# Kernel tuning notes

Hardware: AMD Instinct MI355X
Metric: run time of the kernel (lower is better)

The kernel has to match this reference:

```python
import jax, jax.numpy as jnp
import numpy as np

B, N, FD = 2, 50000, 13
E = 250000
M, H = 128, 128          # message_dim, hidden_dim
EDGE_IN = 2 * FD + 8     # 34
NODE_IN = FD + 2 * M     # 269


def _mlp(x, w1, b1, w2, b2):
    return jnp.tanh(x @ w1 + b1) @ w2 + b2


def setup_inputs() -> dict:
    root = jax.random.key(0)
    k = lambda i: jax.random.fold_in(root, i)

    def lin(i, din, dout):
        w = jax.random.normal(k(i), (din, dout), jnp.float32) * np.float32(1.0 / np.sqrt(din))
        b = jax.random.normal(k(i + 100), (dout,), jnp.float32) * np.float32(0.01)
        return w, b

    ew1, eb1 = lin(1, EDGE_IN, H); ew2, eb2 = lin(2, H, M)      # mlp_edge
    ww1, wb1 = lin(3, EDGE_IN, H); ww2, wb2 = lin(4, H, 1)      # mlp_weight
    xw1, xb1 = lin(5, EDGE_IN, H); xw2, xb2 = lin(6, H, M)      # mlp_edge_world
    yw1, yb1 = lin(7, EDGE_IN, H); yw2, yb2 = lin(8, H, 1)      # mlp_weight_world
    nw1, nb1 = lin(9, NODE_IN, H); nw2, nb2 = lin(10, H, FD)    # mlp_node

    z_h = jax.random.normal(k(20), (B, N, FD), jnp.float32)
    edge_hh = jax.random.randint(k(21), (B, 2, E), 0, N, jnp.int32)
    edge_world = jax.random.randint(k(22), (B, 2, E), 0, N, jnp.int32)
    return dict(z_h=z_h, edge_hh=edge_hh, edge_world=edge_world,
                ew1=ew1, eb1=eb1, ew2=ew2, eb2=eb2,
                ww1=ww1, wb1=wb1, ww2=ww2, wb2=wb2,
                xw1=xw1, xb1=xb1, xw2=xw2, xb2=xb2,
                yw1=yw1, yb1=yb1, yw2=yw2, yb2=yb2,
                nw1=nw1, nb1=nb1, nw2=nw2, nb2=nb2)


def _edge_features(z, s, t):
    # z: (N, FD); s, t: (E,)
    pos, vel = z[:, 0:3], z[:, 3:6]
    diff = pos[s] - pos[t]                               # (E, 3)
    dist = jnp.sum(diff * diff, axis=-1, keepdims=True)  # (E, 1) squared distance
    vxc = jnp.cross(vel[s], vel[t])                      # (E, 3)
    vxn = jnp.linalg.norm(vxc, axis=-1, keepdims=True)   # (E, 1)
    return jnp.concatenate([diff, dist, vxc, vxn], axis=-1)  # (E, 8)


def reference(z_h, edge_hh, edge_world,
              ew1, eb1, ew2, eb2, ww1, wb1, ww2, wb2,
              xw1, xb1, xw2, xb2, yw1, yb1, yw2, yb2,
              nw1, nb1, nw2, nb2):
    n_nodes = z_h.shape[1]

    def per_batch(z, e_hh, e_w):
        # normal edges
        s, t = e_hh[0], e_hh[1]
        inp = jnp.concatenate([z[s], z[t], _edge_features(z, s, t)], axis=-1)  # (E, 34)
        m = _mlp(inp, ew1, eb1, ew2, eb2)                                       # (E, M)
        w = jax.nn.sigmoid(_mlp(inp, ww1, wb1, ww2, wb2))                       # (E, 1)
        agg_h = jnp.zeros((n_nodes, M), z.dtype).at[t].add(w * m)
        # world edges
        sw, tw = e_w[0], e_w[1]
        inpw = jnp.concatenate([z[sw], z[tw], _edge_features(z, sw, tw)], axis=-1)
        mw = _mlp(inpw, xw1, xb1, xw2, xb2)
        ww_ = jax.nn.sigmoid(_mlp(inpw, yw1, yb1, yw2, yb2))
        agg_w = jnp.zeros((n_nodes, M), z.dtype).at[tw].add(ww_ * mw)
        return agg_h, agg_w

    m_agg_h, m_agg_w = jax.vmap(per_batch)(z_h, edge_hh, edge_world)  # (B, N, M) each
    input_node = jnp.concatenate([z_h, m_agg_h, m_agg_w], axis=-1)    # (B, N, 269)
    delta_z_h = _mlp(input_node, nw1, nb1, nw2, nb2)                  # (B, N, 13)
    return delta_z_h
```

## Files before the change

kernel.cpp:

```cpp
#include <hip/hip_runtime.h>
#include <hip/hip_bf16.h>

#define B_   2
#define N_   50000
#define FD_  13
#define E_   250000
#define M_   128
#define H_   128

typedef __attribute__((ext_vector_type(8))) short  short8;
typedef __attribute__((ext_vector_type(8))) __bf16 bf16x8;
typedef __attribute__((ext_vector_type(4))) float  f32x4;
typedef __attribute__((ext_vector_type(8))) unsigned short ushort8;

#define MSG_BYTES  (4ull * E_ * 128 * 2)
#define HIST_BYTES (4ull * N_ * 4)
#define SORT_BYTES (4ull * E_ * 4)
#define OFF_EW1 0u
#define OFF_WW1 8192u
#define OFF_EW2 16384u
#define OFF_XW1 32768u
#define OFF_YW1 40960u
#define OFF_XW2 49152u
#define OFF_NW1 65536u
#define OFF_NW2 102400u

__device__ __forceinline__ float bf2f(unsigned short u) {
    unsigned int v = ((unsigned int)u) << 16;
    return __builtin_bit_cast(float, v);
}
__device__ __forceinline__ unsigned short f2bf(float f) {
    __bf16 h = (__bf16)f;
    return __builtin_bit_cast(unsigned short, h);
}
__device__ __forceinline__ float tanh_fast(float x) {
    float e = __expf(x + x);
    float r = __builtin_amdgcn_rcpf(e + 1.0f);
    return __builtin_fmaf(-2.0f, r, 1.0f);
}
__device__ __forceinline__ float sigmoid_fast(float x) {
    return __builtin_amdgcn_rcpf(1.0f + __expf(-x));
}
__device__ __forceinline__ f32x4 mfma16(short8 a, short8 b, f32x4 c) {
    return __builtin_amdgcn_mfma_f32_16x16x32_bf16(
        __builtin_bit_cast(bf16x8, a), __builtin_bit_cast(bf16x8, b), c, 0, 0, 0);
}

__global__ void prep_kernel(const float* __restrict__ ew1, const float* __restrict__ ww1,
                            const float* __restrict__ ew2, const float* __restrict__ xw1,
                            const float* __restrict__ yw1, const float* __restrict__ xw2,
                            const float* __restrict__ nw1, const float* __restrict__ nw2,
                            unsigned short* __restrict__ fb) {
    int m = blockIdx.y, f = blockIdx.x, l = threadIdx.x;
    const float* src; int K, Nn, KS; unsigned int off;
    switch (m) {
        case 0: src = ew1; K = 34;  Nn = 128; KS = 2; off = OFF_EW1; break;
        case 1: src = ww1; K = 34;  Nn = 128; KS = 2; off = OFF_WW1; break;
        case 2: src = ew2; K = 128; Nn = 128; KS = 4; off = OFF_EW2; break;
        case 3: src = xw1; K = 34;  Nn = 128; KS = 2; off = OFF_XW1; break;
        case 4: src = yw1; K = 34;  Nn = 128; KS = 2; off = OFF_YW1; break;
        case 5: src = xw2; K = 128; Nn = 128; KS = 4; off = OFF_XW2; break;
        case 6: src = nw1; K = 269; Nn = 128; KS = 9; off = OFF_NW1; break;
        default: src = nw2; K = 128; Nn = 13; KS = 4; off = OFF_NW2; break;
    }
    int NT = (Nn + 15) / 16;
    if (f >= KS * NT) return;
    int ks = f / NT, nt = f % NT;
    int n = nt * 16 + (l & 15);
    unsigned short* dst = fb + off + ((unsigned int)f * 64u + (unsigned int)l) * 8u;
    #pragma unroll
    for (int j = 0; j < 8; j++) {
        int k = ks * 32 + ((l >> 4) * 8) + j;
        int kk = k; bool valid = (k < K) && (n < Nn);
        if (m == 6) {
            if (k < 256)      kk = k + 13;
            else if (k < 269) kk = k - 256;
            else              valid = false;
            valid = valid && (n < Nn);
        }
        dst[j] = valid ? f2bf(src[kk * Nn + n]) : (unsigned short)0;
    }
}

__global__ void hist_kernel(const int* __restrict__ ehh, const int* __restrict__ eww,
                            int* __restrict__ hist) {
    int p = blockIdx.y, idx = blockIdx.x * 256 + threadIdx.x;
    if (idx >= E_) return;
    const int* eg = ((p >> 1) ? eww : ehh) + (size_t)(p & 1) * 2 * E_;
    atomicAdd(&hist[p * N_ + eg[E_ + idx]], 1);
}

__global__ void scan_kernel(int* __restrict__ hist) {
    __shared__ int part[1024];
    const int p = blockIdx.x, tid = threadIdx.x;
    int* h = hist + p * N_;
    const int lo = tid * 52;
    int cnt = N_ - lo; if (cnt < 0) cnt = 0; if (cnt > 52) cnt = 52;
    int v[52];
    int sum = 0;
    if (cnt == 52) {
        const int4* src = (const int4*)(h + lo);
        #pragma unroll
        for (int i = 0; i < 13; i++) {
            int4 t = src[i];
            v[4*i] = t.x; v[4*i+1] = t.y; v[4*i+2] = t.z; v[4*i+3] = t.w;
        }
        #pragma unroll
        for (int i = 0; i < 52; i++) sum += v[i];
    } else {
        for (int i = 0; i < cnt; i++) sum += h[lo + i];
    }
    part[tid] = sum;
    __syncthreads();
    for (int off = 1; off < 1024; off <<= 1) {
        int t = (tid >= off) ? part[tid - off] : 0;
        __syncthreads();
        part[tid] += t;
        __syncthreads();
    }
    int excl = (tid == 0) ? 0 : part[tid - 1];
    if (cnt == 52) {
        int4* dst = (int4*)(h + lo);
        #pragma unroll
        for (int i = 0; i < 13; i++) {
            int4 o;
            o.x = excl; excl += v[4*i];
            o.y = excl; excl += v[4*i+1];
            o.z = excl; excl += v[4*i+2];
            o.w = excl; excl += v[4*i+3];
            dst[i] = o;
        }
    } else {
        for (int i = 0; i < cnt; i++) { int t = h[lo + i]; h[lo + i] = excl; excl += t; }
    }
}

__global__ void scatter_kernel(const int* __restrict__ ehh, const int* __restrict__ eww,
                               int* __restrict__ hist, unsigned int* __restrict__ sorted) {
    int p = blockIdx.y, idx = blockIdx.x * 256 + threadIdx.x;
    if (idx >= E_) return;
    const int* eg = ((p >> 1) ? eww : ehh) + (size_t)(p & 1) * 2 * E_;
    int s = eg[idx];
    int t = eg[E_ + idx];
    int pos = atomicAdd(&hist[p * N_ + t], 1);
    sorted[(size_t)p * E_ + pos] = (unsigned int)s | ((unsigned int)t << 16);
}

__launch_bounds__(256, 3)
__global__ void edge_kernel_msg(const float* __restrict__ z,
                                const unsigned int* __restrict__ sorted,
                                const unsigned short* __restrict__ fb,
                                unsigned short* __restrict__ msg,
                                const float* __restrict__ eb1, const float* __restrict__ wb1,
                                const float* __restrict__ ww2, const float* __restrict__ wb2,
                                const float* __restrict__ eb2,
                                const float* __restrict__ xb1, const float* __restrict__ yb1,
                                const float* __restrict__ yw2, const float* __restrict__ yb2,
                                const float* __restrict__ xb2) {
    __shared__ alignas(16) unsigned short Abuf[128][48];
    __shared__ alignas(16) unsigned short Hbuf[128][136];
    __shared__ float w_acc[128];

    const int tid  = threadIdx.x;
    const int lane = tid & 63, wv = tid >> 6, quad = lane >> 4, c = lane & 15;
    const int pass = blockIdx.y, b = pass & 1, set = pass >> 1;
    const int ebase = blockIdx.x * 128;

    const float* zb = z + (size_t)b * N_ * FD_;
    unsigned short* msgp = msg + (size_t)pass * E_ * 128;

    const short8* Fm1 = (const short8*)(fb + (set ? OFF_XW1 : OFF_EW1));
    const short8* Fw1 = (const short8*)(fb + (set ? OFF_YW1 : OFF_WW1));
    const short8* Fm2 = (const short8*)(fb + (set ? OFF_XW2 : OFF_EW2));
    const float* B1m = set ? xb1 : eb1;
    const float* B1w = set ? yb1 : wb1;
    const float* B2m = set ? xb2 : eb2;
    const float* Wv2 = set ? yw2 : ww2;
    const float wbias = (set ? yb2 : wb2)[0];

    const int nt0 = wv * 2;
    short8 bm[2][2], bw[2][2], b2f[2][4];
    float bias1m[2], bias1w[2], bias2m[2], w2v[2];
    #pragma unroll
    for (int i = 0; i < 2; i++) {
        int nt = nt0 + i, n = nt * 16 + c;
        #pragma unroll
        for (int ks = 0; ks < 2; ks++) { bm[i][ks] = Fm1[(ks * 8 + nt) * 64 + lane];
                                         bw[i][ks] = Fw1[(ks * 8 + nt) * 64 + lane]; }
        #pragma unroll
        for (int ks = 0; ks < 4; ks++) { b2f[i][ks] = Fm2[(ks * 8 + nt) * 64 + lane]; }
        bias1m[i] = B1m[n]; bias1w[i] = B1w[n];
        bias2m[i] = B2m[n]; w2v[i] = Wv2[n];
    }

    if (tid < 128) {
        const int e = tid;
        int sp = ebase + e; if (sp >= E_) sp = E_ - 1;
        unsigned int st = sorted[(size_t)pass * E_ + sp];
        int s = (int)(st & 0xffffu), t = (int)(st >> 16);
        w_acc[e] = 0.0f;
        const float* zs = zb + (size_t)s * 13;
        const float* zt = zb + (size_t)t * 13;
        float fs[13], ft[13];
        __builtin_memcpy(fs, zs, 13 * sizeof(float));
        __builtin_memcpy(ft, zt, 13 * sizeof(float));
        float d0 = fs[0] - ft[0], d1 = fs[1] - ft[1], d2 = fs[2] - ft[2];
        float dist = d0 * d0 + d1 * d1 + d2 * d2;
        float c0 = fs[4] * ft[5] - fs[5] * ft[4];
        float c1 = fs[5] * ft[3] - fs[3] * ft[5];
        float c2 = fs[3] * ft[4] - fs[4] * ft[3];
        float vxn = sqrtf(c0 * c0 + c1 * c1 + c2 * c2);
        unsigned short row[40];
        #pragma unroll
        for (int j = 0; j < 13; j++) { row[j] = f2bf(fs[j]); row[13 + j] = f2bf(ft[j]); }
        row[26] = f2bf(d0); row[27] = f2bf(d1); row[28] = f2bf(d2); row[29] = f2bf(dist);
        row[30] = f2bf(c0); row[31] = f2bf(c1); row[32] = f2bf(c2); row[33] = f2bf(vxn);
        #pragma unroll
        for (int j = 34; j < 40; j++) row[j] = 0;
        #pragma unroll
        for (int v = 0; v < 5; v++) {
            short8 sv;
            #pragma unroll
            for (int j = 0; j < 8; j++) sv[j] = (short)row[v * 8 + j];
            *((short8*)&Abuf[e][v * 8]) = sv;
        }
    }
    __syncthreads();

    #pragma unroll 1
    for (int rt = 0; rt < 8; rt++) {
        const unsigned short* ar = &Abuf[rt * 16 + c][0];
        short8 a0 = *((const short8*)(ar + quad * 8));
        short8 a1 = {};
        if (quad == 0) a1 = *((const short8*)(ar + 32));
        float wpart[4] = {0.f, 0.f, 0.f, 0.f};
        #pragma unroll
        for (int i = 0; i < 2; i++) {
            f32x4 accm = {bias1m[i], bias1m[i], bias1m[i], bias1m[i]};
            f32x4 accw = {bias1w[i], bias1w[i], bias1w[i], bias1w[i]};
            accm = mfma16(a0, bm[i][0], accm);
            accm = mfma16(a1, bm[i][1], accm);
            accw = mfma16(a0, bw[i][0], accw);
            accw = mfma16(a1, bw[i][1], accw);
            int n = (nt0 + i) * 16 + c;
            #pragma unroll
            for (int r = 0; r < 4; r++) {
                Hbuf[rt * 16 + quad * 4 + r][n] = f2bf(tanh_fast(accm[r]));
                wpart[r] += tanh_fast(accw[r]) * w2v[i];
            }
        }
        #pragma unroll
        for (int r = 0; r < 4; r++) {
            float v = wpart[r];
            v += __shfl_xor(v, 1); v += __shfl_xor(v, 2);
            v += __shfl_xor(v, 4); v += __shfl_xor(v, 8);
            if (c == r) atomicAdd(&w_acc[rt * 16 + quad * 4 + r], v);
        }
    }
    __syncthreads();
    if (tid < 128) w_acc[tid] = sigmoid_fast(w_acc[tid] + wbias);
    __syncthreads();

    #pragma unroll 1
    for (int rt = 0; rt < 8; rt++) {
        const unsigned short* hr = &Hbuf[rt * 16 + c][0];
        short8 h0 = *((const short8*)(hr + quad * 8));
        short8 h1 = *((const short8*)(hr + 32 + quad * 8));
        short8 h2 = *((const short8*)(hr + 64 + quad * 8));
        short8 h3 = *((const short8*)(hr + 96 + quad * 8));
        const int elq = rt * 16 + quad * 4;
        const float g0 = w_acc[elq + 0], g1 = w_acc[elq + 1];
        const float g2 = w_acc[elq + 2], g3 = w_acc[elq + 3];
        #pragma unroll
        for (int i = 0; i < 2; i++) {
            f32x4 acc = {bias2m[i], bias2m[i], bias2m[i], bias2m[i]};
            acc = mfma16(h0, b2f[i][0], acc);
            acc = mfma16(h1, b2f[i][1], acc);
            acc = mfma16(h2, b2f[i][2], acc);
            acc = mfma16(h3, b2f[i][3], acc);
            const int n = (nt0 + i) * 16 + c;
            const float gv[4] = {g0, g1, g2, g3};
            #pragma unroll
            for (int r = 0; r < 4; r++) {
                int e = elq + r;
                if (ebase + e < E_)
                    msgp[(size_t)(ebase + e) * 128 + n] = f2bf(acc[r] * gv[r]);
            }
        }
    }
}

__launch_bounds__(256, 4)
__global__ void node_fused(const float* __restrict__ z,
                           const unsigned short* __restrict__ msg,
                           const int* __restrict__ hist,
                           const unsigned short* __restrict__ fb,
                           const float* __restrict__ nb1,
                           const float* __restrict__ nb2,
                           float* __restrict__ out) {
    __shared__ alignas(16) unsigned short Abuf[16][296];
    __shared__ alignas(16) unsigned short Hbuf[16][136];

    const int tid  = threadIdx.x;
    const int lane = tid & 63, wv = tid >> 6, quad = lane >> 4, c = lane & 15;
    const int g0 = blockIdx.x * 16;

    {
        const int nl = tid >> 4;
        const int part = tid & 15;
        const int g = g0 + nl;
        const int b = (g >= N_) ? 1 : 0;
        const int t = g - b * N_;
        #pragma unroll
        for (int s = 0; s < 2; s++) {
            const int p = s * 2 + b;
            const int end   = hist[p * N_ + t];
            const int start = (t > 0) ? hist[p * N_ + t - 1] : 0;
            float acc[8];
            #pragma unroll
            for (int k = 0; k < 8; k++) acc[k] = 0.f;
            const unsigned short* mp = msg + (size_t)p * E_ * 128 + part * 8;
            int j = start;
            for (; j + 8 <= end; j += 8) {
                ushort8 m[8];
                #pragma unroll
                for (int q = 0; q < 8; q++)
                    m[q] = *(const ushort8*)(mp + (size_t)(j + q) * 128);
                #pragma unroll
                for (int k = 0; k < 8; k++)
                    acc[k] += ((bf2f(m[0][k]) + bf2f(m[1][k])) + (bf2f(m[2][k]) + bf2f(m[3][k])))
                            + ((bf2f(m[4][k]) + bf2f(m[5][k])) + (bf2f(m[6][k]) + bf2f(m[7][k])));
            }
            for (; j + 2 <= end; j += 2) {
                ushort8 m0 = *(const ushort8*)(mp + (size_t)(j + 0) * 128);
                ushort8 m1 = *(const ushort8*)(mp + (size_t)(j + 1) * 128);
                #pragma unroll
                for (int k = 0; k < 8; k++) acc[k] += bf2f(m0[k]) + bf2f(m1[k]);
            }
            for (; j < end; j++) {
                ushort8 m = *(const ushort8*)(mp + (size_t)j * 128);
                #pragma unroll
                for (int k = 0; k < 8; k++) acc[k] += bf2f(m[k]);
            }
            ushort8 u;
            #pragma unroll
            for (int k = 0; k < 8; k++) u[k] = f2bf(acc[k]);
            *((ushort8*)&Abuf[nl][s * 128 + part * 8]) = u;
        }
    }
    for (int j = tid; j < 16 * 13; j += 256) {
        int nl = j / 13, k = j % 13;
        Abuf[nl][256 + k] = f2bf(z[(size_t)(g0 + nl) * 13 + k]);
    }
    for (int j = tid; j < 16 * 19; j += 256) {
        int nl = j / 19, k = j % 19;
        Abuf[nl][269 + k] = 0;
    }
    __syncthreads();

    {
        const short8* F1 = (const short8*)(fb + OFF_NW1);
        const int nt0 = wv * 2;
        const float b1a = nb1[nt0 * 16 + c];
        const float b1b = nb1[(nt0 + 1) * 16 + c];
        f32x4 acc0 = {b1a, b1a, b1a, b1a};
        f32x4 acc1 = {b1b, b1b, b1b, b1b};
        #pragma unroll
        for (int ks = 0; ks < 9; ks++) {
            short8 a = *((const short8*)(&Abuf[c][0] + ks * 32 + quad * 8));
            acc0 = mfma16(a, F1[(ks * 8 + nt0) * 64 + lane], acc0);
            acc1 = mfma16(a, F1[(ks * 8 + nt0 + 1) * 64 + lane], acc1);
        }
        #pragma unroll
        for (int r = 0; r < 4; r++) {
            Hbuf[quad * 4 + r][nt0 * 16 + c]       = f2bf(tanh_fast(acc0[r]));
            Hbuf[quad * 4 + r][(nt0 + 1) * 16 + c] = f2bf(tanh_fast(acc1[r]));
        }
    }
    __syncthreads();

    if (wv == 0) {
        const short8* F2 = (const short8*)(fb + OFF_NW2);
        const float bias2 = (c < 13) ? nb2[c] : 0.0f;
        f32x4 acc = {bias2, bias2, bias2, bias2};
        #pragma unroll
        for (int ks = 0; ks < 4; ks++) {
            short8 h = *((const short8*)(&Hbuf[c][0] + ks * 32 + quad * 8));
            acc = mfma16(h, F2[ks * 64 + lane], acc);
        }
        #pragma unroll
        for (int r = 0; r < 4; r++) {
            int g = g0 + quad * 4 + r;
            if (c < 13) out[(size_t)g * 13 + c] = acc[r];
        }
    }
}

extern "C" void kernel_launch(void* const* d_in, const int* in_sizes, int n_in,
                              void* d_out, int out_size, void* d_ws, size_t ws_size,
                              hipStream_t stream) {
    const float* z   = (const float*)d_in[0];
    const int* ehh   = (const int*)d_in[1];
    const int* eww   = (const int*)d_in[2];
    const float* ew1 = (const float*)d_in[3];
    const float* eb1 = (const float*)d_in[4];
    const float* ew2 = (const float*)d_in[5];
    const float* eb2 = (const float*)d_in[6];
    const float* ww1 = (const float*)d_in[7];
    const float* wb1 = (const float*)d_in[8];
    const float* ww2 = (const float*)d_in[9];
    const float* wb2 = (const float*)d_in[10];
    const float* xw1 = (const float*)d_in[11];
    const float* xb1 = (const float*)d_in[12];
    const float* xw2 = (const float*)d_in[13];
    const float* xb2 = (const float*)d_in[14];
    const float* yw1 = (const float*)d_in[15];
    const float* yb1 = (const float*)d_in[16];
    const float* yw2 = (const float*)d_in[17];
    const float* yb2 = (const float*)d_in[18];
    const float* nw1 = (const float*)d_in[19];
    const float* nb1 = (const float*)d_in[20];
    const float* nw2 = (const float*)d_in[21];
    const float* nb2 = (const float*)d_in[22];

    unsigned short* msg = (unsigned short*)d_ws;
    int* hist   = (int*)((char*)d_ws + MSG_BYTES);
    unsigned int* sorted = (unsigned int*)((char*)d_ws + MSG_BYTES + HIST_BYTES);
    unsigned short* frag = (unsigned short*)((char*)d_ws + MSG_BYTES + HIST_BYTES + SORT_BYTES);

    hipMemsetAsync(hist, 0, HIST_BYTES, stream);
    prep_kernel<<<dim3(72, 8), 64, 0, stream>>>(ew1, ww1, ew2, xw1, yw1, xw2, nw1, nw2, frag);
    hist_kernel<<<dim3((E_ + 255) / 256, 4), 256, 0, stream>>>(ehh, eww, hist);
    scan_kernel<<<4, 1024, 0, stream>>>(hist);
    scatter_kernel<<<dim3((E_ + 255) / 256, 4), 256, 0, stream>>>(ehh, eww, hist, sorted);
    edge_kernel_msg<<<dim3((E_ + 127) / 128, 4), 256, 0, stream>>>(
        z, sorted, frag, msg,
        eb1, wb1, ww2, wb2, eb2,
        xb1, yb1, yw2, yb2, xb2);
    node_fused<<<(B_ * N_) / 16, 256, 0, stream>>>(
        z, msg, hist, frag, nb1, nb2, (float*)d_out);
}
```

Before: 436.1 us.

## Aggregate edge messages via float atomics instead of materializing per-edge messages

The edge kernel no longer writes a bf16 message per edge for the node kernel to reduce by CSR segment. It now adds weighted messages straight into an fp32 per-node aggregation buffer with atomicAdd, first merging consecutive rows that share a target (edges are sorted by target). The node kernel just reads the aggregated rows. This avoids writing and re-reading the large message buffer, at the cost of zeroing a 100MB fp32 buffer, atomic contention, and nondeterministic summation order.

```diff
diff --git a/kernel.cpp b/kernel.cpp
--- a/kernel.cpp
+++ b/kernel.cpp
@@ -13,7 +13,7 @@
 typedef __attribute__((ext_vector_type(4))) float  f32x4;
 typedef __attribute__((ext_vector_type(8))) unsigned short ushort8;
 
-#define MSG_BYTES  (4ull * E_ * 128 * 2)
+#define AGG_BYTES  (4ull * N_ * 128 * 4)
 #define HIST_BYTES (4ull * N_ * 4)
 #define SORT_BYTES (4ull * E_ * 4)
 #define OFF_EW1 0u
@@ -147,10 +147,10 @@
 }
 
 __launch_bounds__(256, 3)
-__global__ void edge_kernel_msg(const float* __restrict__ z,
+__global__ void edge_kernel_agg(const float* __restrict__ z,
                                 const unsigned int* __restrict__ sorted,
                                 const unsigned short* __restrict__ fb,
-                                unsigned short* __restrict__ msg,
+                                float* __restrict__ agg,
                                 const float* __restrict__ eb1, const float* __restrict__ wb1,
                                 const float* __restrict__ ww2, const float* __restrict__ wb2,
                                 const float* __restrict__ eb2,
@@ -160,6 +160,7 @@
     __shared__ alignas(16) unsigned short Abuf[128][48];
     __shared__ alignas(16) unsigned short Hbuf[128][136];
     __shared__ float w_acc[128];
+    __shared__ int   tgt_s[128];
 
     const int tid  = threadIdx.x;
     const int lane = tid & 63, wv = tid >> 6, quad = lane >> 4, c = lane & 15;
@@ -167,7 +168,7 @@
     const int ebase = blockIdx.x * 128;
 
     const float* zb = z + (size_t)b * N_ * FD_;
-    unsigned short* msgp = msg + (size_t)pass * E_ * 128;
+    float* aggp = agg + (size_t)pass * N_ * 128;
 
     const short8* Fm1 = (const short8*)(fb + (set ? OFF_XW1 : OFF_EW1));
     const short8* Fw1 = (const short8*)(fb + (set ? OFF_YW1 : OFF_WW1));
@@ -195,9 +196,12 @@
 
     if (tid < 128) {
         const int e = tid;
-        int sp = ebase + e; if (sp >= E_) sp = E_ - 1;
+        int sp = ebase + e;
+        const bool valid = (sp < E_);
+        if (!valid) sp = E_ - 1;
         unsigned int st = sorted[(size_t)pass * E_ + sp];
         int s = (int)(st & 0xffffu), t = (int)(st >> 16);
+        tgt_s[e] = valid ? t : -1;
         w_acc[e] = 0.0f;
         const float* zs = zb + (size_t)s * 13;
         const float* zt = zb + (size_t)t * 13;
@@ -269,8 +273,8 @@
         short8 h2 = *((const short8*)(hr + 64 + quad * 8));
         short8 h3 = *((const short8*)(hr + 96 + quad * 8));
         const int elq = rt * 16 + quad * 4;
-        const float g0 = w_acc[elq + 0], g1 = w_acc[elq + 1];
-        const float g2 = w_acc[elq + 2], g3 = w_acc[elq + 3];
+        const int   tg[4] = {tgt_s[elq], tgt_s[elq + 1], tgt_s[elq + 2], tgt_s[elq + 3]};
+        const float gv[4] = {w_acc[elq], w_acc[elq + 1], w_acc[elq + 2], w_acc[elq + 3]};
         #pragma unroll
         for (int i = 0; i < 2; i++) {
             f32x4 acc = {bias2m[i], bias2m[i], bias2m[i], bias2m[i]};
@@ -279,21 +283,26 @@
             acc = mfma16(h2, b2f[i][2], acc);
             acc = mfma16(h3, b2f[i][3], acc);
             const int n = (nt0 + i) * 16 + c;
-            const float gv[4] = {g0, g1, g2, g3};
+            int   tp = tg[0];
+            float va = acc[0] * gv[0];
             #pragma unroll
-            for (int r = 0; r < 4; r++) {
-                int e = elq + r;
-                if (ebase + e < E_)
-                    msgp[(size_t)(ebase + e) * 128 + n] = f2bf(acc[r] * gv[r]);
+            for (int r = 1; r < 4; r++) {
+                float v = acc[r] * gv[r];
+                if (tg[r] == tp) {
+                    va += v;
+                } else {
+                    if (tp >= 0) atomicAdd(&aggp[(size_t)tp * 128 + n], va);
+                    tp = tg[r]; va = v;
+                }
             }
+            if (tp >= 0) atomicAdd(&aggp[(size_t)tp * 128 + n], va);
         }
     }
 }
 
 __launch_bounds__(256, 4)
 __global__ void node_fused(const float* __restrict__ z,
-                           const unsigned short* __restrict__ msg,
-                           const int* __restrict__ hist,
+                           const float* __restrict__ agg,
                            const unsigned short* __restrict__ fb,
                            const float* __restrict__ nb1,
                            const float* __restrict__ nb2,
@@ -313,38 +322,12 @@
         const int t = g - b * N_;
         #pragma unroll
         for (int s = 0; s < 2; s++) {
-            const int p = s * 2 + b;
-            const int end   = hist[p * N_ + t];
-            const int start = (t > 0) ? hist[p * N_ + t - 1] : 0;
-            float acc[8];
-            #pragma unroll
-            for (int k = 0; k < 8; k++) acc[k] = 0.f;
-            const unsigned short* mp = msg + (size_t)p * E_ * 128 + part * 8;
-            int j = start;
-            for (; j + 8 <= end; j += 8) {
-                ushort8 m[8];
-                #pragma unroll
-                for (int q = 0; q < 8; q++)
-                    m[q] = *(const ushort8*)(mp + (size_t)(j + q) * 128);
-                #pragma unroll
-                for (int k = 0; k < 8; k++)
-                    acc[k] += ((bf2f(m[0][k]) + bf2f(m[1][k])) + (bf2f(m[2][k]) + bf2f(m[3][k])))
-                            + ((bf2f(m[4][k]) + bf2f(m[5][k])) + (bf2f(m[6][k]) + bf2f(m[7][k])));
-            }
-            for (; j + 2 <= end; j += 2) {
-                ushort8 m0 = *(const ushort8*)(mp + (size_t)(j + 0) * 128);
-                ushort8 m1 = *(const ushort8*)(mp + (size_t)(j + 1) * 128);
-                #pragma unroll
-                for (int k = 0; k < 8; k++) acc[k] += bf2f(m0[k]) + bf2f(m1[k]);
-            }
-            for (; j < end; j++) {
-                ushort8 m = *(const ushort8*)(mp + (size_t)j * 128);
-                #pragma unroll
-                for (int k = 0; k < 8; k++) acc[k] += bf2f(m[k]);
-            }
+            const float* ap = agg + ((size_t)(s * 2 + b) * N_ + t) * 128 + part * 8;
+            f32x4 v0 = *(const f32x4*)(ap);
+            f32x4 v1 = *(const f32x4*)(ap + 4);
             ushort8 u;
             #pragma unroll
-            for (int k = 0; k < 8; k++) u[k] = f2bf(acc[k]);
+            for (int k = 0; k < 4; k++) { u[k] = f2bf(v0[k]); u[4 + k] = f2bf(v1[k]); }
             *((ushort8*)&Abuf[nl][s * 128 + part * 8]) = u;
         }
     }
@@ -423,20 +406,20 @@
     const float* nw2 = (const float*)d_in[21];
     const float* nb2 = (const float*)d_in[22];
 
-    unsigned short* msg = (unsigned short*)d_ws;
-    int* hist   = (int*)((char*)d_ws + MSG_BYTES);
-    unsigned int* sorted = (unsigned int*)((char*)d_ws + MSG_BYTES + HIST_BYTES);
-    unsigned short* frag = (unsigned short*)((char*)d_ws + MSG_BYTES + HIST_BYTES + SORT_BYTES);
-
-    hipMemsetAsync(hist, 0, HIST_BYTES, stream);
+    float* agg  = (float*)d_ws;
+    int* hist   = (int*)((char*)d_ws + AGG_BYTES);
+    unsigned int* sorted = (unsigned int*)((char*)d_ws + AGG_BYTES + HIST_BYTES);
+    unsigned short* frag = (unsigned short*)((char*)d_ws + AGG_BYTES + HIST_BYTES + SORT_BYTES);
+
+    hipMemsetAsync(d_ws, 0, AGG_BYTES + HIST_BYTES, stream);
     prep_kernel<<<dim3(72, 8), 64, 0, stream>>>(ew1, ww1, ew2, xw1, yw1, xw2, nw1, nw2, frag);
     hist_kernel<<<dim3((E_ + 255) / 256, 4), 256, 0, stream>>>(ehh, eww, hist);
     scan_kernel<<<4, 1024, 0, stream>>>(hist);
     scatter_kernel<<<dim3((E_ + 255) / 256, 4), 256, 0, stream>>>(ehh, eww, hist, sorted);
-    edge_kernel_msg<<<dim3((E_ + 127) / 128, 4), 256, 0, stream>>>(
-        z, sorted, frag, msg,
+    edge_kernel_agg<<<dim3((E_ + 127) / 128, 4), 256, 0, stream>>>(
+        z, sorted, frag, agg,
         eb1, wb1, ww2, wb2, eb2,
         xb1, yb1, yw2, yb2, xb2);
     node_fused<<<(B_ * N_) / 16, 256, 0, stream>>>(
-        z, msg, hist, frag, nb1, nb2, (float*)d_out);
-}
+        z, agg, frag, nb1, nb2, (float*)d_out);
+}
```

Result: slower. 555.3 us (+27.3%).
